# Kernel optimization log

Hardware: AMD Instinct MI355X
Metric: run time of the kernel (lower is better)

Reference implementation:

```python
import jax, jax.numpy as jnp
import numpy as np
from jax import lax

SCORE_THR = 0.1
IOU_THR = 0.3
NUM_CLASSES = 80
MAX_COORD = 4096.0  # class offset for class-aware NMS (boxes live in [0, ~1100])


def setup_inputs() -> dict:
    key = jax.random.key(0)
    bs, n = 4, 4096
    k1, k2, k3, k4 = jax.random.split(key, 4)
    # realistic boxes: centers in [0,1024], w/h in [10,210]
    cxcy = jax.random.uniform(k1, (bs, n, 2), minval=0.0, maxval=1024.0)
    wh = jax.random.uniform(k2, (bs, n, 2), minval=10.0, maxval=210.0)
    x1y1 = cxcy - wh * 0.5
    x2y2 = cxcy + wh * 0.5
    scores = jax.random.uniform(k3, (bs, n, 1), minval=0.0, maxval=1.0)
    cls = jax.random.randint(k4, (bs, n, 1), 0, NUM_CLASSES).astype(jnp.float32)
    batch_preds = jnp.concatenate([x1y1, x2y2, scores, cls], axis=-1)  # [bs, n, 6]
    return {"batch_preds": batch_preds}


def _iou_matrix(boxes):
    # boxes: [N, 4] (x1, y1, x2, y2) -> pairwise IoU [N, N]
    x1, y1, x2, y2 = boxes[:, 0], boxes[:, 1], boxes[:, 2], boxes[:, 3]
    area = (x2 - x1) * (y2 - y1)
    ix1 = jnp.maximum(x1[:, None], x1[None, :])
    iy1 = jnp.maximum(y1[:, None], y1[None, :])
    ix2 = jnp.minimum(x2[:, None], x2[None, :])
    iy2 = jnp.minimum(y2[:, None], y2[None, :])
    inter = jnp.maximum(ix2 - ix1, 0.0) * jnp.maximum(iy2 - iy1, 0.0)
    return inter / (area[:, None] + area[None, :] - inter + 1e-9)


def _nms_image(preds):
    # preds: [N, 6]. Returns preds zeroed where not kept (fixed-shape mask NMS).
    n = preds.shape[0]
    boxes, scores, cls = preds[:, :4], preds[:, 4], preds[:, 5]
    valid = scores >= SCORE_THR
    # class-aware trick == per-class NMS: offset boxes by class so cross-class IoU = 0
    obox = boxes + (cls * MAX_COORD)[:, None]
    order = jnp.argsort(-jnp.where(valid, scores, -jnp.inf))
    sboxes = obox[order]
    svalid = valid[order]
    iou = _iou_matrix(sboxes)  # [N, N]
    idxs = jnp.arange(n)

    def body(suppressed, inp):
        iou_row, v_i, i = inp
        keep_i = v_i & jnp.logical_not(suppressed[i])
        suppressed = suppressed | (keep_i & (iou_row > IOU_THR) & (idxs > i))
        return suppressed, keep_i

    _, keep_sorted = lax.scan(body, jnp.zeros((n,), bool), (iou, svalid, idxs))
    keep = jnp.zeros((n,), bool).at[order].set(keep_sorted)
    return preds * keep[:, None].astype(preds.dtype)


def reference(batch_preds):
    # Fixed-shape formulation of score filtering + per-class greedy NMS:
    # suppressed / below-threshold rows are zeroed instead of removed.
    return jax.vmap(_nms_image)(batch_preds)
```

## Files before the change

### kernel.cpp

```cpp
#include <hip/hip_runtime.h>
#include <hip/hip_bf16.h>

typedef unsigned long long u64;

#define BS 4
#define NBOX 4096
#define NCLS 80
#define CPB 4
#define NBLK 20
#define THREADS 256
#define SLICE 205
#define CAPC 128
#define SCORE_THR 0.1f
#define IOU_THR 0.3f
#define MAX_COORD 4096.0f

__global__ __launch_bounds__(THREADS) void k_nms_all(const float* __restrict__ preds,
                                                     float* __restrict__ out) {
    __shared__ unsigned mem[CPB][CAPC];
    __shared__ unsigned scnt[CPB];
    __shared__ u64 skey[CPB][CAPC];
    __shared__ float4 sbxs[CPB][CAPC];
    __shared__ unsigned sidxs[CPB][CAPC];

    const int img = blockIdx.y;
    const int g = blockIdx.x;
    const int t = threadIdx.x;
    const int w = t >> 6;
    const int lane = t & 63;
    const float* P = preds + (size_t)img * NBOX * 6;
    float* O = out + (size_t)img * NBOX * 6;

    if (t < CPB) scnt[t] = 0;
    __syncthreads();

    const int sbeg = g * SLICE;
    const int send = min(NBOX, sbeg + SLICE);
#pragma unroll
    for (int r = 0; r < NBOX / THREADS; ++r) {
        int m = t + r * THREADS;
        float2 sc = *(const float2*)(P + (size_t)m * 6 + 4);
        if (sc.x >= SCORE_THR) {
            int lc = (int)sc.y - g * CPB;
            if (lc >= 0 && lc < CPB) {
                unsigned slot = atomicAdd(&scnt[lc], 1u);
                if (slot < CAPC) mem[lc][slot] = (unsigned)m;
            }
        } else if (m >= sbeg && m < send) {
            float2* W2 = (float2*)(O + (size_t)m * 6);
            float2 z = make_float2(0.f, 0.f);
            W2[0] = z; W2[1] = z; W2[2] = z;
        }
    }
    __syncthreads();

    const int s = (int)min(scnt[w], (unsigned)CAPC);

    u64 key[2];
    float4 bx2[2] = {make_float4(0,0,0,0), make_float4(0,0,0,0)};
    unsigned oi[2] = {0, 0};
#pragma unroll
    for (int r = 0; r < 2; ++r) {
        int m = lane + 64 * r;
        key[r] = ~0ull;
        if (m < s) {
            unsigned e = mem[w][m];
            oi[r] = e;
            const float* R = P + (size_t)e * 6;
            float x1 = R[0], y1 = R[1], x2 = R[2], y2 = R[3], sc = R[4], cl = R[5];
            float off = cl * MAX_COORD;
            bx2[r] = make_float4(x1 + off, y1 + off, x2 + off, y2 + off);
            unsigned u = __float_as_uint(sc);
            u = (u & 0x80000000u) ? ~u : (u | 0x80000000u);
            key[r] = ((u64)(~u) << 32) | (u64)e;
        }
        skey[w][m] = key[r];
    }
    __syncthreads();

    int rank[2] = {0, 0};
    for (int j = 0; j < s; ++j) {
        u64 kj = skey[w][j];
        rank[0] += (kj < key[0]);
        rank[1] += (kj < key[1]);
    }
    __syncthreads();
#pragma unroll
    for (int r = 0; r < 2; ++r) {
        int m = lane + 64 * r;
        if (m < s) { sbxs[w][rank[r]] = bx2[r]; sidxs[w][rank[r]] = oi[r]; }
    }
    __syncthreads();

    float4 cb[2];
    float ca[2];
    bool removed[2];
#pragma unroll
    for (int r = 0; r < 2; ++r) {
        int c = lane + 64 * r;
        removed[r] = (c >= s);
        cb[r] = make_float4(0.f, 0.f, 0.f, 0.f);
        ca[r] = 0.f;
        if (c < s) {
            cb[r] = sbxs[w][c];
            ca[r] = (cb[r].z - cb[r].x) * (cb[r].w - cb[r].y);
        }
    }
    for (int i = 0; i < s; ++i) {
        float4 rb = sbxs[w][i];
        u64 mA = __ballot(removed[0]);
        u64 mB = __ballot(removed[1]);
        u64 m = (i < 64) ? mA : mB;
        bool kept = !((m >> (i & 63)) & 1ull);
        if (kept) {
            float ra = (rb.z - rb.x) * (rb.w - rb.y);
#pragma unroll
            for (int r = 0; r < 2; ++r) {
                int c = lane + 64 * r;
                if (c > i && !removed[r]) {
                    float ix1 = fmaxf(rb.x, cb[r].x), iy1 = fmaxf(rb.y, cb[r].y);
                    float ix2 = fminf(rb.z, cb[r].z), iy2 = fminf(rb.w, cb[r].w);
                    float iw = fmaxf(ix2 - ix1, 0.f), ih = fmaxf(iy2 - iy1, 0.f);
                    float inter = iw * ih;
                    float iou = inter / (ra + ca[r] - inter + 1e-9f);
                    if (iou > IOU_THR) removed[r] = true;
                }
            }
        }
    }

#pragma unroll
    for (int r = 0; r < 2; ++r) {
        int c = lane + 64 * r;
        if (c < s) {
            unsigned e = sidxs[w][c];
            const float2* R2 = (const float2*)(P + (size_t)e * 6);
            float2* W2 = (float2*)(O + (size_t)e * 6);
            if (!removed[r]) {
                W2[0] = R2[0]; W2[1] = R2[1]; W2[2] = R2[2];
            } else {
                float2 z = make_float2(0.f, 0.f);
                W2[0] = z; W2[1] = z; W2[2] = z;
            }
        }
    }
}

extern "C" void kernel_launch(void* const* d_in, const int* in_sizes, int n_in,
                              void* d_out, int out_size, void* d_ws, size_t ws_size,
                              hipStream_t stream) {
    const float* preds = (const float*)d_in[0];
    float* out = (float*)d_out;
    k_nms_all<<<dim3(NBLK, BS), THREADS, 0, stream>>>(preds, out);
}
```

Baseline: 78.05 us.

## Precompute IoU suppression bitmasks then run serial greedy scan on masks

Replaces the per-iteration greedy loop, which needed a ballot and a data-dependent branch each step, with two phases. First each wave computes full upper-triangular IoU overlap bitmasks for every sorted box and stores them in shared memory. Then a cheap serial scan over the 64-bit masks resolves the greedy suppression. Block shape also changes to 1024 threads handling 16 classes per block with 5 blocks per image. This removes the serial dependency from the IoU arithmetic but adds shared memory and computes IoUs for rows that would have been suppressed anyway.

```diff
diff --git a/kernel.cpp b/kernel.cpp
--- a/kernel.cpp
+++ b/kernel.cpp
@@ -6,10 +6,10 @@
 #define BS 4
 #define NBOX 4096
 #define NCLS 80
-#define CPB 4
-#define NBLK 20
-#define THREADS 256
-#define SLICE 205
+#define CPB 16
+#define NBLK 5
+#define THREADS 1024
+#define SLICE 820
 #define CAPC 128
 #define SCORE_THR 0.1f
 #define IOU_THR 0.3f
@@ -20,6 +20,7 @@
     __shared__ unsigned mem[CPB][CAPC];
     __shared__ unsigned scnt[CPB];
     __shared__ u64 skey[CPB][CAPC];
+    __shared__ u64 smaskB[CPB][CAPC];
     __shared__ float4 sbxs[CPB][CAPC];
     __shared__ unsigned sidxs[CPB][CAPC];
 
@@ -66,11 +67,11 @@
         if (m < s) {
             unsigned e = mem[w][m];
             oi[r] = e;
-            const float* R = P + (size_t)e * 6;
-            float x1 = R[0], y1 = R[1], x2 = R[2], y2 = R[3], sc = R[4], cl = R[5];
-            float off = cl * MAX_COORD;
-            bx2[r] = make_float4(x1 + off, y1 + off, x2 + off, y2 + off);
-            unsigned u = __float_as_uint(sc);
+            const float2* R2 = (const float2*)(P + (size_t)e * 6);
+            float2 p01 = R2[0], p23 = R2[1], p45 = R2[2];
+            float off = p45.y * MAX_COORD;
+            bx2[r] = make_float4(p01.x + off, p01.y + off, p23.x + off, p23.y + off);
+            unsigned u = __float_as_uint(p45.x);
             u = (u & 0x80000000u) ? ~u : (u | 0x80000000u);
             key[r] = ((u64)(~u) << 32) | (u64)e;
         }
@@ -94,11 +95,9 @@
 
     float4 cb[2];
     float ca[2];
-    bool removed[2];
 #pragma unroll
     for (int r = 0; r < 2; ++r) {
         int c = lane + 64 * r;
-        removed[r] = (c >= s);
         cb[r] = make_float4(0.f, 0.f, 0.f, 0.f);
         ca[r] = 0.f;
         if (c < s) {
@@ -106,28 +105,40 @@
             ca[r] = (cb[r].z - cb[r].x) * (cb[r].w - cb[r].y);
         }
     }
+
     for (int i = 0; i < s; ++i) {
         float4 rb = sbxs[w][i];
-        u64 mA = __ballot(removed[0]);
-        u64 mB = __ballot(removed[1]);
-        u64 m = (i < 64) ? mA : mB;
-        bool kept = !((m >> (i & 63)) & 1ull);
-        if (kept) {
-            float ra = (rb.z - rb.x) * (rb.w - rb.y);
+        float ra = (rb.z - rb.x) * (rb.w - rb.y);
+        bool p0 = false, p1 = false;
 #pragma unroll
-            for (int r = 0; r < 2; ++r) {
-                int c = lane + 64 * r;
-                if (c > i && !removed[r]) {
-                    float ix1 = fmaxf(rb.x, cb[r].x), iy1 = fmaxf(rb.y, cb[r].y);
-                    float ix2 = fminf(rb.z, cb[r].z), iy2 = fminf(rb.w, cb[r].w);
-                    float iw = fmaxf(ix2 - ix1, 0.f), ih = fmaxf(iy2 - iy1, 0.f);
-                    float inter = iw * ih;
-                    float iou = inter / (ra + ca[r] - inter + 1e-9f);
-                    if (iou > IOU_THR) removed[r] = true;
-                }
+        for (int r = 0; r < 2; ++r) {
+            int c = lane + 64 * r;
+            if (c > i && c < s) {
+                float ix1 = fmaxf(rb.x, cb[r].x), iy1 = fmaxf(rb.y, cb[r].y);
+                float ix2 = fminf(rb.z, cb[r].z), iy2 = fminf(rb.w, cb[r].w);
+                float iw = fmaxf(ix2 - ix1, 0.f), ih = fmaxf(iy2 - iy1, 0.f);
+                float inter = iw * ih;
+                float iou = inter / (ra + ca[r] - inter + 1e-9f);
+                bool hit = iou > IOU_THR;
+                if (r == 0) p0 = hit; else p1 = hit;
             }
         }
+        u64 mA = __ballot(p0);
+        u64 mB = __ballot(p1);
+        if (lane == 0) { skey[w][i] = mA; smaskB[w][i] = mB; }
     }
+    __syncthreads();
+
+    u64 remA = 0, remB = 0;
+    for (int i = 0; i < s; ++i) {
+        u64 rA = skey[w][i];
+        u64 rB = smaskB[w][i];
+        bool irem = (i < 64) ? (((remA >> i) & 1ull) != 0ull)
+                             : (((remB >> (i - 64)) & 1ull) != 0ull);
+        if (!irem) { remA |= rA; remB |= rB; }
+    }
+    bool removed[2] = { ((remA >> lane) & 1ull) != 0ull,
+                        ((remB >> lane) & 1ull) != 0ull };
 
 #pragma unroll
     for (int r = 0; r < 2; ++r) {
```

Measured after the change: 78.65 us. Within noise of the previous version (+0.8%).
